# Optimization experiments

Measured on AMD Instinct MI355X. Metric: run time of the kernel, lower is better.

The kernel has to match this reference:

```python
import jax, jax.numpy as jnp
import numpy as np

B, T, E, QKV, H = 2, 2048, 1024, 1024, 16
DH = QKV // H
R_LAYER = 2

def rmsnorm(x):
    eps = jnp.finfo(x.dtype).eps
    return x * jax.lax.rsqrt(jnp.mean(x * x, axis=-1, keepdims=True) + eps)

def w_norm(w, n):
    # scale whole matrix so its (unbiased) std matches n**-0.5
    std = jnp.std(w, ddof=1)
    return w * (n ** -0.5 / (std + 1e-8))

def rotary(x, cos, sin):
    d = x.shape[-1] // 2
    x1, x2 = x[..., :d], x[..., d:]
    return jnp.concatenate([x1 * cos + x2 * sin, -x1 * sin + x2 * cos], axis=-1)

def w_split(w):
    w_qkv = w[:3 * QKV]                               # (3*QKV, E)
    w_sw = w[3 * QKV:5 * QKV].reshape(2 * E, QKV)     # (2*E, QKV)
    w_out = w[5 * QKV:]                               # (E, E)
    return w_qkv, w_sw, w_out

def aft(x, w_qkv):
    qkv = rmsnorm(x) @ w_qkv.T                        # (B,T,3*QKV)
    q, k, v = jnp.split(qkv, 3, axis=-1)
    q, k = rmsnorm(q), rmsnorm(k)
    wexp = jnp.exp(k)
    kv_c = jnp.cumsum(wexp * v, axis=1)
    w_c = jnp.cumsum(wexp, axis=1)
    y = jax.nn.sigmoid(q) * kv_c / (w_c + 1e-6)
    return x, y

def tea(x, cos, sin, w_qkv):
    qkv = (rmsnorm(x) @ w_qkv.T).reshape(B, T, H, 3 * DH)
    q, k, v = jnp.split(qkv, 3, axis=-1)              # each (B,T,H,DH)
    q, k = rotary(q, cos, sin), rotary(k, cos, sin)
    q, k = rmsnorm(q), rmsnorm(k)
    q = q.transpose(0, 2, 1, 3)                       # (B,H,T,DH)
    k = k.transpose(0, 2, 1, 3)
    v = v.transpose(0, 2, 1, 3)
    scores = jnp.einsum('bhqd,bhkd->bhqk', q, k) * DH ** -0.5
    mask = jnp.tril(jnp.ones((T, T), dtype=bool))
    scores = jnp.where(mask, scores, -jnp.inf)
    att = jax.nn.softmax(scores, axis=-1)
    y = jnp.einsum('bhqk,bhkd->bhqd', att, v)
    return x, y.transpose(0, 2, 1, 3).reshape(B, T, QKV)

def swiglu(x, y, w_sw, w_out, ret_oa=True):
    uv = y @ w_sw.T                                   # (B,T,2*E)
    u, v = jnp.split(uv, 2, axis=-1)
    out = x + (u * jax.nn.silu(v)) @ w_out.T
    if not ret_oa:
        return out
    o = rmsnorm(u.reshape(B * T, -1))
    a = v.reshape(B * T, -1)
    oa = jax.nn.softmax((o.T @ a) * E ** -0.5, axis=-1)  # (E,E)
    return out, oa

def setup_inputs():
    key = jax.random.key(0)
    k1, k2 = jax.random.split(key)
    x = jax.random.normal(k1, (B, T, E), dtype=jnp.float32)
    s = 3 ** 0.5 * E ** -0.5
    w = jax.random.uniform(k2, (5 * QKV + E, E), dtype=jnp.float32, minval=-s, maxval=s)
    half = DH // 2
    inv_freq = 1.0 / (10000.0 ** (jnp.arange(half, dtype=jnp.float32) / half))
    freqs = jnp.outer(jnp.arange(T, dtype=jnp.float32), inv_freq)  # (T, half)
    cos = jnp.cos(freqs)[:, None, :]                  # (T,1,half) broadcasts over (B,T,H,half)
    sin = jnp.sin(freqs)[:, None, :]
    return {"x": x, "w": w, "cos": cos, "sin": sin}

def reference(x, w, cos, sin):
    for i in range(R_LAYER):
        w_qkv, w_sw, w_out = w_split(w)
        w_qkv = w_norm(w_qkv, E)
        w_sw = w_norm(w_sw, QKV)
        w_out = w_norm(w_out, E)
        if (i + 1) % 4 == 0:
            x, y = tea(x, cos, sin, w_qkv)
        else:
            x, y = aft(x, w_qkv)
        x, oa = swiglu(x, y, w_sw, w_out, ret_oa=True)
        # RetentionMechanism.forward: hypernetwork weight mixing
        wT = w_norm(w @ oa, 5 * QKV + E)
        w = wT * jax.nn.silu(w) + w
    w_qkv, w_sw, w_out = w_split(w)                   # note: no w_norm on final split (matches source)
    x, y = tea(x, cos, sin, w_qkv)
    return swiglu(x, y, w_sw, w_out, ret_oa=False)
```

## Files before the change

kernel.cpp:

```cpp
#include <hip/hip_runtime.h>
#include <hip/hip_bf16.h>
#include <math.h>

#define TPB 256

constexpr int Bc = 2, Tc = 2048, Ec = 1024, QKVc = 1024, Hc = 16, DHc = 64;
constexpr long BT = (long)Bc * Tc;
constexpr int WR = 5 * QKVc + Ec;
constexpr float F32_EPS = 1.1920928955078125e-07f;
constexpr int NCH = 64, CHL = Tc / NCH;

typedef __attribute__((ext_vector_type(8))) short short8;
typedef __attribute__((ext_vector_type(4))) float f32x4;

__device__ __forceinline__ unsigned short f2bu(float f) {
    union { __hip_bfloat16 h; unsigned short u; } c; c.h = __float2bfloat16(f); return c.u;
}
__device__ __forceinline__ float bu2f(unsigned short u) {
    union { __hip_bfloat16 h; unsigned short u; } c; c.u = u; return __bfloat162float(c.h);
}
__device__ __forceinline__ float ldval(const float* p) { return *p; }
__device__ __forceinline__ float ldval(const unsigned short* p) { return bu2f(*p); }

__device__ __forceinline__ void gload_lds16(const void* g, void* l) {
    __builtin_amdgcn_global_load_lds((const __attribute__((address_space(1))) void*)g,
                                     (__attribute__((address_space(3))) void*)l, 16, 0, 0);
}

template<int CTRL>
__device__ __forceinline__ float dppf(float x) {
    union { float f; int i; } a, b;
    a.f = x;
    b.i = __builtin_amdgcn_update_dpp(0, a.i, CTRL, 0xF, 0xF, true);
    return b.f;
}
__device__ __forceinline__ float max16(float v) {
    v = fmaxf(v, dppf<0xB1>(v));
    v = fmaxf(v, dppf<0x4E>(v));
    v = fmaxf(v, dppf<0x124>(v));
    v = fmaxf(v, dppf<0x128>(v));
    return v;
}
__device__ __forceinline__ float sum16(float v) {
    v += dppf<0xB1>(v);
    v += dppf<0x4E>(v);
    v += dppf<0x124>(v);
    v += dppf<0x128>(v);
    return v;
}

__global__ void k_std_partial3(const float* __restrict__ w, float* __restrict__ out) {
    __shared__ float ls[TPB], lss[TPB];
    int seg = blockIdx.y;
    long base = (seg == 0) ? 0L : (seg == 1 ? 3072L * 1024 : 5120L * 1024);
    long n    = (seg == 0) ? 3072L * 1024 : (seg == 1 ? 2048L * 1024 : 1024L * 1024);
    const float* p = w + base;
    float s = 0.f, ss = 0.f;
    for (long i = (long)blockIdx.x * TPB + threadIdx.x; i < n; i += 256L * TPB) {
        float v = p[i]; s += v; ss += v * v;
    }
    ls[threadIdx.x] = s; lss[threadIdx.x] = ss; __syncthreads();
    for (int o = 128; o > 0; o >>= 1) {
        if (threadIdx.x < o) { ls[threadIdx.x] += ls[threadIdx.x + o]; lss[threadIdx.x] += lss[threadIdx.x + o]; }
        __syncthreads();
    }
    if (threadIdx.x == 0) { out[seg * 512 + blockIdx.x] = ls[0]; out[seg * 512 + 256 + blockIdx.x] = lss[0]; }
}

__global__ void k_std_final3(const float* __restrict__ part, float* __restrict__ scales) {
    __shared__ float ls[TPB], lss[TPB];
    for (int seg = 0; seg < 3; ++seg) {
        ls[threadIdx.x] = part[seg * 512 + threadIdx.x];
        lss[threadIdx.x] = part[seg * 512 + 256 + threadIdx.x];
        __syncthreads();
        for (int o = 128; o > 0; o >>= 1) {
            if (threadIdx.x < o) { ls[threadIdx.x] += ls[threadIdx.x + o]; lss[threadIdx.x] += lss[threadIdx.x + o]; }
            __syncthreads();
        }
        if (threadIdx.x == 0) {
            float n = (seg == 0) ? 3145728.0f : (seg == 1 ? 2097152.0f : 1048576.0f);
            float var = (lss[0] - ls[0] * ls[0] / n) / (n - 1.0f);
            scales[seg] = 0.03125f / (sqrtf(fmaxf(var, 0.0f)) + 1e-8f);
        }
        __syncthreads();
    }
}

__global__ void k_std_partial(const float* __restrict__ p, long n, float* __restrict__ out) {
    __shared__ float ls[TPB], lss[TPB];
    float s = 0.f, ss = 0.f;
    for (long i = (long)blockIdx.x * TPB + threadIdx.x; i < n; i += (long)gridDim.x * TPB) {
        float v = p[i]; s += v; ss += v * v;
    }
    ls[threadIdx.x] = s; lss[threadIdx.x] = ss; __syncthreads();
    for (int o = 128; o > 0; o >>= 1) {
        if (threadIdx.x < o) { ls[threadIdx.x] += ls[threadIdx.x + o]; lss[threadIdx.x] += lss[threadIdx.x + o]; }
        __syncthreads();
    }
    if (threadIdx.x == 0) { out[blockIdx.x] = ls[0]; out[gridDim.x + blockIdx.x] = lss[0]; }
}

__global__ void k_std_final(const float* __restrict__ part, float n, float rs, float* __restrict__ scale) {
    __shared__ float ls[TPB], lss[TPB];
    ls[threadIdx.x] = part[threadIdx.x];
    lss[threadIdx.x] = part[TPB + threadIdx.x];
    __syncthreads();
    for (int o = 128; o > 0; o >>= 1) {
        if (threadIdx.x < o) { ls[threadIdx.x] += ls[threadIdx.x + o]; lss[threadIdx.x] += lss[threadIdx.x + o]; }
        __syncthreads();
    }
    if (threadIdx.x == 0) {
        float var = (lss[0] - ls[0] * ls[0] / n) / (n - 1.0f);
        scale[0] = rs / (sqrtf(fmaxf(var, 0.0f)) + 1e-8f);
    }
}

__global__ void k_rms_qk(unsigned short* __restrict__ qkv) {
    __shared__ float red[TPB];
    int bid = blockIdx.x;
    long row = bid >> 1; int half = bid & 1;
    unsigned short* p = qkv + row * 3072 + half * 1024;
    ushort4 v = *(const ushort4*)(p + threadIdx.x * 4);
    float f0 = bu2f(v.x), f1 = bu2f(v.y), f2 = bu2f(v.z), f3 = bu2f(v.w);
    red[threadIdx.x] = f0 * f0 + f1 * f1 + f2 * f2 + f3 * f3;
    __syncthreads();
    for (int o = 128; o > 0; o >>= 1) {
        if (threadIdx.x < o) red[threadIdx.x] += red[threadIdx.x + o];
        __syncthreads();
    }
    float sc = rsqrtf(red[0] / 1024.0f + F32_EPS);
    ushort4 o4; o4.x = f2bu(f0 * sc); o4.y = f2bu(f1 * sc); o4.z = f2bu(f2 * sc); o4.w = f2bu(f3 * sc);
    *(ushort4*)(p + threadIdx.x * 4) = o4;
}

__global__ void k_rms1024b(const float* __restrict__ in, unsigned short* __restrict__ out, long ldin, long ldout) {
    __shared__ float red[TPB];
    long row = blockIdx.x;
    float4 v = *(const float4*)(in + row * ldin + threadIdx.x * 4);
    float ss = v.x * v.x + v.y * v.y + v.z * v.z + v.w * v.w;
    red[threadIdx.x] = ss; __syncthreads();
    for (int o = 128; o > 0; o >>= 1) {
        if (threadIdx.x < o) red[threadIdx.x] += red[threadIdx.x + o];
        __syncthreads();
    }
    float sc = rsqrtf(red[0] / 1024.0f + F32_EPS);
    ushort4 o4; o4.x = f2bu(v.x * sc); o4.y = f2bu(v.y * sc); o4.z = f2bu(v.z * sc); o4.w = f2bu(v.w * sc);
    *(ushort4*)(out + row * ldout + threadIdx.x * 4) = o4;
}

__global__ void k_cast_bf16(const float* __restrict__ in, unsigned short* __restrict__ out, long n4) {
    long i = (long)blockIdx.x * TPB + threadIdx.x;
    if (i >= n4) return;
    float4 v = *(const float4*)(in + i * 4);
    ushort4 o; o.x = f2bu(v.x); o.y = f2bu(v.y); o.z = f2bu(v.z); o.w = f2bu(v.w);
    *(ushort4*)(out + i * 4) = o;
}

template<typename TI>
__global__ void k_tcast(const TI* __restrict__ in, long ldi, long sIn,
                        unsigned short* __restrict__ out, long ldo, long sOut,
                        const float* __restrict__ rowscale) {
    __shared__ float tile[64][65];
    const TI* ip = in + (long)blockIdx.z * sIn;
    unsigned short* op = out + (long)blockIdx.z * sOut;
    int r0 = blockIdx.y * 64, c0 = blockIdx.x * 64;
    int tid = threadIdx.x;
    int rr = tid >> 4, cc = (tid & 15) * 4;
    #pragma unroll
    for (int u = 0; u < 4; ++u) {
        int r = rr + u * 16;
        float sc = rowscale ? rowscale[r0 + r] : 1.0f;
        #pragma unroll
        for (int j = 0; j < 4; ++j)
            tile[r][cc + j] = ldval(ip + (long)(r0 + r) * ldi + c0 + cc + j) * sc;
    }
    __syncthreads();
    #pragma unroll
    for (int u = 0; u < 4; ++u) {
        int c = rr + u * 16;
        ushort4 o;
        o.x = f2bu(tile[cc + 0][c]); o.y = f2bu(tile[cc + 1][c]);
        o.z = f2bu(tile[cc + 2][c]); o.w = f2bu(tile[cc + 3][c]);
        *(ushort4*)(op + (long)(c0 + c) * ldo + r0 + cc) = o;
    }
}

__global__ void k_tcast2(const unsigned short* __restrict__ uv, const float* __restrict__ uscale,
                         unsigned short* __restrict__ t1, unsigned short* __restrict__ t2) {
    __shared__ float tile[64][65];
    int z = blockIdx.z;
    const unsigned short* ip = uv + (z ? 1024 : 0);
    unsigned short* op = z ? t2 : t1;
    int r0 = blockIdx.y * 64, c0 = blockIdx.x * 64;
    int tid = threadIdx.x;
    int rr = tid >> 4, cc = (tid & 15) * 4;
    #pragma unroll
    for (int u = 0; u < 4; ++u) {
        int r = rr + u * 16;
        float sc = z ? 1.0f : uscale[r0 + r];
        ushort4 v = *(const ushort4*)(ip + (long)(r0 + r) * 2048 + c0 + cc);
        tile[r][cc + 0] = bu2f(v.x) * sc; tile[r][cc + 1] = bu2f(v.y) * sc;
        tile[r][cc + 2] = bu2f(v.z) * sc; tile[r][cc + 3] = bu2f(v.w) * sc;
    }
    __syncthreads();
    #pragma unroll
    for (int u = 0; u < 4; ++u) {
        int c = rr + u * 16;
        ushort4 o;
        o.x = f2bu(tile[cc + 0][c]); o.y = f2bu(tile[cc + 1][c]);
        o.z = f2bu(tile[cc + 2][c]); o.w = f2bu(tile[cc + 3][c]);
        *(ushort4*)(op + (long)(c0 + c) * 4096 + r0 + cc) = o;
    }
}

template<int WRITE_BF16>
__global__ __launch_bounds__(256)
void k_bgemm(int K,
             const unsigned short* __restrict__ A, int lda, long sA,
             const unsigned short* __restrict__ B, int ldb, long sB,
             void* __restrict__ C, int ldc, long sCi, long sSplit, int nsplit,
             const float* __restrict__ scale_ptr, float fscale,
             const float* __restrict__ addp, int ldadd) {
    __shared__ unsigned short Asl[128 * 64];
    __shared__ unsigned short Bsl[128 * 64];
    int bz = blockIdx.z;
    int batch = bz, sp = 0;
    if (nsplit > 1) { batch = bz / nsplit; sp = bz - batch * nsplit; }
    int m0 = blockIdx.y * 128, n0 = blockIdx.x * 128;
    const unsigned short* Ap = A + (long)batch * sA + (long)sp * K;
    const unsigned short* Bp = B + (long)batch * sB + (long)sp * K;
    int tid = threadIdx.x, lane = tid & 63, wave = tid >> 6;
    int wr = wave >> 1, wc = wave & 1;
    f32x4 acc[4][4] = {};
    for (int k0 = 0; k0 < K; k0 += 64) {
        #pragma unroll
        for (int cc = 0; cc < 4; ++cc) {
            int bu = (wave * 4 + cc) * 64;
            int uidx = bu + lane;
            int r = uidx >> 3, slot = uidx & 7;
            int gu = slot ^ (r & 7);
            gload_lds16(Ap + (long)(m0 + r) * lda + k0 + gu * 8, Asl + bu * 8);
        }
        #pragma unroll
        for (int cc = 0; cc < 4; ++cc) {
            int bu = (wave * 4 + cc) * 64;
            int uidx = bu + lane;
            int r = uidx >> 3, slot = uidx & 7;
            int gu = slot ^ (r & 7);
            gload_lds16(Bp + (long)(n0 + r) * ldb + k0 + gu * 8, Bsl + bu * 8);
        }
        __syncthreads();
        #pragma unroll
        for (int ksub = 0; ksub < 2; ++ksub) {
            short8 av[4], bv[4];
            #pragma unroll
            for (int m = 0; m < 4; ++m) {
                int r = wr * 64 + m * 16 + (lane & 15);
                int slot = (ksub * 4 + (lane >> 4)) ^ (r & 7);
                av[m] = *(const short8*)(Asl + r * 64 + slot * 8);
            }
            #pragma unroll
            for (int n = 0; n < 4; ++n) {
                int r = wc * 64 + n * 16 + (lane & 15);
                int slot = (ksub * 4 + (lane >> 4)) ^ (r & 7);
                bv[n] = *(const short8*)(Bsl + r * 64 + slot * 8);
            }
            #pragma unroll
            for (int m = 0; m < 4; ++m)
                #pragma unroll
                for (int n = 0; n < 4; ++n)
                    acc[m][n] = __builtin_amdgcn_mfma_f32_16x16x32_bf16(av[m], bv[n], acc[m][n], 0, 0, 0);
        }
        __syncthreads();
    }
    float s = fscale * (scale_ptr ? scale_ptr[0] : 1.0f);
    long cbase = (long)batch * sCi + (long)sp * sSplit;
    int row0 = m0 + wr * 64, col0 = n0 + wc * 64 + (lane & 15);
    int rbase = (lane >> 4) * 4;
    #pragma unroll
    for (int m = 0; m < 4; ++m)
        #pragma unroll
        for (int i = 0; i < 4; ++i) {
            long row = row0 + m * 16 + rbase + i;
            #pragma unroll
            for (int n = 0; n < 4; ++n) {
                long col = col0 + n * 16;
                float v = acc[m][n][i] * s;
                if (addp) v += addp[row * (long)ldadd + col];
                long idx = cbase + row * ldc + col;
                if (WRITE_BF16) ((unsigned short*)C)[idx] = f2bu(v);
                else ((float*)C)[idx] = v;
            }
        }
}

__global__ __launch_bounds__(256)
void k_flash_split(const unsigned short* __restrict__ hq, const unsigned short* __restrict__ hk,
                   const unsigned short* __restrict__ hvT,
                   unsigned short* __restrict__ opart, float* __restrict__ mpart, float* __restrict__ lpart) {
    __shared__ unsigned short P_lds[4][32 * 136];
    int lane = threadIdx.x & 63, wave = threadIdx.x >> 6;
    unsigned short* P = P_lds[wave];
    int g = lane >> 4, c = lane & 15;
    unsigned bid = blockIdx.x;
    unsigned bswz = (bid & 7) * 160 + (bid >> 3);
    unsigned gi = bswz * 4 + wave;
    unsigned bh = gi / 160, itr = gi % 160;
    int item = 159 - (int)itr;
    int strip, chunk;
    if (item < 16)      { strip = item;                 chunk = 0; }
    else if (item < 48) { strip = 16 + (item - 16) / 2; chunk = (item - 16) & 1; }
    else if (item < 96) { strip = 32 + (item - 48) / 3; chunk = (item - 48) % 3; }
    else                { strip = 48 + (item - 96) / 4; chunk = (item - 96) & 3; }
    int q0 = strip * 32;
    int nt = (q0 + 32 + 127) >> 7;
    int ti0 = chunk * 4;
    int ti1 = ti0 + 4 < nt ? ti0 + 4 : nt;
    const unsigned short* qb = hq + (long)bh * Tc * 64;
    const unsigned short* kb = hk + (long)bh * Tc * 64;
    const unsigned short* vtb = hvT + (long)bh * 64 * Tc;

    short8 qf[2][2];
    #pragma unroll
    for (int mf = 0; mf < 2; ++mf)
        #pragma unroll
        for (int ks = 0; ks < 2; ++ks)
            qf[mf][ks] = *(const short8*)(qb + (long)(q0 + mf * 16 + c) * 64 + ks * 32 + g * 8);

    f32x4 o_acc[2][4] = {};
    float m_run[2][4], lpp[2][4];
    #pragma unroll
    for (int mf = 0; mf < 2; ++mf)
        #pragma unroll
        for (int i = 0; i < 4; ++i) { m_run[mf][i] = -3.0e38f; lpp[mf][i] = 0.f; }

    for (int ti = ti0; ti < ti1; ++ti) {
        int kt = ti * 128;
        short8 vf[4][4];
        #pragma unroll
        for (int ks2 = 0; ks2 < 4; ++ks2)
            #pragma unroll
            for (int df = 0; df < 4; ++df)
                vf[ks2][df] = *(const short8*)(vtb + (long)(df * 16 + c) * Tc + kt + ks2 * 32 + g * 8);
        f32x4 s_acc[2][8] = {};
        #pragma unroll
        for (int ks = 0; ks < 2; ++ks) {
            short8 kf[8];
            #pragma unroll
            for (int nf = 0; nf < 8; ++nf)
                kf[nf] = *(const short8*)(kb + (long)(kt + nf * 16 + c) * 64 + ks * 32 + g * 8);
            #pragma unroll
            for (int mf = 0; mf < 2; ++mf)
                #pragma unroll
                for (int nf = 0; nf < 8; ++nf)
                    s_acc[mf][nf] = __builtin_amdgcn_mfma_f32_16x16x32_bf16(qf[mf][ks], kf[nf], s_acc[mf][nf], 0, 0, 0);
        }
        if (ti == nt - 1) {
            #pragma unroll
            for (int mf = 0; mf < 2; ++mf)
                #pragma unroll
                for (int nf = 0; nf < 8; ++nf)
                    #pragma unroll
                    for (int i = 0; i < 4; ++i)
                        if ((kt + nf * 16 + c) > (q0 + mf * 16 + g * 4 + i)) s_acc[mf][nf][i] = -1.0e30f;
        }
        float pm[2][4];
        #pragma unroll
        for (int mf = 0; mf < 2; ++mf)
            #pragma unroll
            for (int i = 0; i < 4; ++i) {
                float a = fmaxf(fmaxf(s_acc[mf][0][i], s_acc[mf][1][i]),
                                fmaxf(s_acc[mf][2][i], s_acc[mf][3][i]));
                float b = fmaxf(fmaxf(s_acc[mf][4][i], s_acc[mf][5][i]),
                                fmaxf(s_acc[mf][6][i], s_acc[mf][7][i]));
                pm[mf][i] = max16(fmaxf(a, b));
            }
        float mg = 0.f;
        #pragma unroll
        for (int mf = 0; mf < 2; ++mf)
            #pragma unroll
            for (int i = 0; i < 4; ++i) {
                pm[mf][i] *= 0.125f;
                mg = fmaxf(mg, pm[mf][i] - m_run[mf][i]);
            }
        if (__any(mg > 8.0f)) {
            #pragma unroll
            for (int mf = 0; mf < 2; ++mf)
                #pragma unroll
                for (int i = 0; i < 4; ++i) {
                    float mn = fmaxf(m_run[mf][i], pm[mf][i]);
                    float corr = __expf(m_run[mf][i] - mn);
                    m_run[mf][i] = mn;
                    lpp[mf][i] *= corr;
                    #pragma unroll
                    for (int df = 0; df < 4; ++df) o_acc[mf][df][i] *= corr;
                }
        }
        #pragma unroll
        for (int mf = 0; mf < 2; ++mf)
            #pragma unroll
            for (int nf = 0; nf < 8; ++nf)
                #pragma unroll
                for (int i = 0; i < 4; ++i) {
                    float p = __expf(fmaf(s_acc[mf][nf][i], 0.125f, -m_run[mf][i]));
                    P[(mf * 16 + g * 4 + i) * 136 + nf * 16 + c] = f2bu(p);
                    lpp[mf][i] += p;
                }
        #pragma unroll
        for (int ks2 = 0; ks2 < 4; ++ks2) {
            short8 pa[2];
            #pragma unroll
            for (int mf = 0; mf < 2; ++mf)
                pa[mf] = *(const short8*)(P + (mf * 16 + c) * 136 + ks2 * 32 + g * 8);
            #pragma unroll
            for (int mf = 0; mf < 2; ++mf)
                #pragma unroll
                for (int df = 0; df < 4; ++df)
                    o_acc[mf][df] = __builtin_amdgcn_mfma_f32_16x16x32_bf16(pa[mf], vf[ks2][df], o_acc[mf][df], 0, 0, 0);
        }
    }
    #pragma unroll
    for (int mf = 0; mf < 2; ++mf)
        #pragma unroll
        for (int i = 0; i < 4; ++i)
            lpp[mf][i] = sum16(lpp[mf][i]);
    long pbase = (long)(bh * 160 + item);
    #pragma unroll
    for (int mf = 0; mf < 2; ++mf)
        #pragma unroll
        for (int i = 0; i < 4; ++i) {
            int row_l = mf * 16 + g * 4 + i;
            #pragma unroll
            for (int df = 0; df < 4; ++df)
                opart[pbase * 2048 + row_l * 64 + df * 16 + c] = f2bu(o_acc[mf][df][i]);
            if (c == 0) {
                mpart[pbase * 32 + row_l] = m_run[mf][i];
                lpart[pbase * 32 + row_l] = lpp[mf][i];
            }
        }
}

__global__ __launch_bounds__(256)
void k_flash_merge(const unsigned short* __restrict__ opart, const float* __restrict__ mpart,
                   const float* __restrict__ lpart, unsigned short* __restrict__ yout) {
    int bs = blockIdx.x;
    int bh = bs >> 6, strip = bs & 63;
    int b = bh >> 4, h = bh & 15;
    int np, base;
    if (strip < 16)      { np = 1; base = strip; }
    else if (strip < 32) { np = 2; base = 16 + (strip - 16) * 2; }
    else if (strip < 48) { np = 3; base = 48 + (strip - 32) * 3; }
    else                 { np = 4; base = 96 + (strip - 48) * 4; }
    long p0 = (long)(bh * 160 + base);
    int tid = threadIdx.x;
    int r = tid >> 3, c0 = (tid & 7) * 8;
    float M = -3.0e38f;
    for (int p = 0; p < np; ++p) M = fmaxf(M, mpart[(p0 + p) * 32 + r]);
    float L = 0.f;
    float acc[8] = {};
    for (int p = 0; p < np; ++p) {
        float sc = __expf(mpart[(p0 + p) * 32 + r] - M);
        L += lpart[(p0 + p) * 32 + r] * sc;
        const unsigned short* op = opart + (p0 + p) * 2048 + r * 64 + c0;
        ushort4 a = *(const ushort4*)op;
        ushort4 bq = *(const ushort4*)(op + 4);
        acc[0] += bu2f(a.x) * sc; acc[1] += bu2f(a.y) * sc;
        acc[2] += bu2f(a.z) * sc; acc[3] += bu2f(a.w) * sc;
        acc[4] += bu2f(bq.x) * sc; acc[5] += bu2f(bq.y) * sc;
        acc[6] += bu2f(bq.z) * sc; acc[7] += bu2f(bq.w) * sc;
    }
    float inv = 1.0f / L;
    long row = (long)b * Tc + strip * 32 + r;
    unsigned short* yp = yout + row * 1024 + h * 64 + c0;
    ushort4 o1, o2;
    o1.x = f2bu(acc[0] * inv); o1.y = f2bu(acc[1] * inv); o1.z = f2bu(acc[2] * inv); o1.w = f2bu(acc[3] * inv);
    o2.x = f2bu(acc[4] * inv); o2.y = f2bu(acc[5] * inv); o2.z = f2bu(acc[6] * inv); o2.w = f2bu(acc[7] * inv);
    *(ushort4*)yp = o1;
    *(ushort4*)(yp + 4) = o2;
}

__global__ void k_aft_p1(const unsigned short* __restrict__ qkv, float* __restrict__ cw, float* __restrict__ cs) {
    int id = blockIdx.x * TPB + threadIdx.x;
    int bc = id & 2047, ch = id >> 11;
    int b = bc >> 10, c = bc & 1023;
    const unsigned short* base = qkv + ((long)(b * Tc + ch * CHL)) * 3072 + c;
    float sw = 0.f, sv = 0.f;
    for (int i = 0; i < CHL; ++i) {
        float k = bu2f(base[1024]), v = bu2f(base[2048]);
        float e = __expf(k);
        sw += e; sv += e * v;
        base += 3072;
    }
    cw[ch * 2048 + bc] = sw; cs[ch * 2048 + bc] = sv;
}

__global__ void k_aft_p3(const unsigned short* __restrict__ qkv, const float* __restrict__ cw,
                         const float* __restrict__ cs, unsigned short* __restrict__ y) {
    int id = blockIdx.x * TPB + threadIdx.x;
    int bc = id & 2047, ch = id >> 11;
    int b = bc >> 10, c = bc & 1023;
    float aw = 0.f, av = 0.f;
    for (int cc = 0; cc < ch; ++cc) { aw += cw[cc * 2048 + bc]; av += cs[cc * 2048 + bc]; }
    long t0 = (long)b * Tc + ch * CHL;
    const unsigned short* base = qkv + t0 * 3072 + c;
    unsigned short* yp = y + t0 * 1024 + c;
    for (int i = 0; i < CHL; ++i) {
        float q = bu2f(base[0]), k = bu2f(base[1024]), v = bu2f(base[2048]);
        float e = __expf(k);
        av += e * v; aw += e;
        float sig = 1.0f / (1.0f + __expf(-q));
        yp[0] = f2bu(sig * av / (aw + 1e-6f));
        base += 3072; yp += 1024;
    }
}

__global__ void k_silu_rms(const unsigned short* __restrict__ uv, unsigned short* __restrict__ g,
                           float* __restrict__ rs) {
    __shared__ float red[TPB];
    long row = blockIdx.x;
    const unsigned short* up = uv + row * 2048;
    ushort4 u4 = *(const ushort4*)(up + threadIdx.x * 4);
    ushort4 v4 = *(const ushort4*)(up + 1024 + threadIdx.x * 4);
    float u0 = bu2f(u4.x), u1 = bu2f(u4.y), u2 = bu2f(u4.z), u3 = bu2f(u4.w);
    float v0 = bu2f(v4.x), v1 = bu2f(v4.y), v2 = bu2f(v4.z), v3 = bu2f(v4.w);
    ushort4 o;
    o.x = f2bu(u0 * v0 / (1.f + __expf(-v0)));
    o.y = f2bu(u1 * v1 / (1.f + __expf(-v1)));
    o.z = f2bu(u2 * v2 / (1.f + __expf(-v2)));
    o.w = f2bu(u3 * v3 / (1.f + __expf(-v3)));
    *(ushort4*)(g + row * 1024 + threadIdx.x * 4) = o;
    red[threadIdx.x] = u0 * u0 + u1 * u1 + u2 * u2 + u3 * u3;
    __syncthreads();
    for (int off = 128; off > 0; off >>= 1) {
        if (threadIdx.x < off) red[threadIdx.x] += red[threadIdx.x + off];
        __syncthreads();
    }
    if (threadIdx.x == 0) rs[row] = rsqrtf(red[0] / 1024.0f + F32_EPS);
}

__global__ void k_silu_gate(const unsigned short* __restrict__ uv, unsigned short* __restrict__ g, long n4) {
    long i = (long)blockIdx.x * TPB + threadIdx.x;
    if (i >= n4) return;
    long r = i >> 8, c4 = i & 255;
    ushort4 u4 = *(const ushort4*)(uv + r * 2048 + c4 * 4);
    ushort4 v4 = *(const ushort4*)(uv + r * 2048 + 1024 + c4 * 4);
    float u0 = bu2f(u4.x), u1 = bu2f(u4.y), u2 = bu2f(u4.z), u3 = bu2f(u4.w);
    float v0 = bu2f(v4.x), v1 = bu2f(v4.y), v2 = bu2f(v4.z), v3 = bu2f(v4.w);
    ushort4 o;
    o.x = f2bu(u0 * v0 / (1.f + __expf(-v0)));
    o.y = f2bu(u1 * v1 / (1.f + __expf(-v1)));
    o.z = f2bu(u2 * v2 / (1.f + __expf(-v2)));
    o.w = f2bu(u3 * v3 / (1.f + __expf(-v3)));
    *(ushort4*)(g + r * 1024 + c4 * 4) = o;
}

__global__ void k_wupdate(float* __restrict__ wout, const float* __restrict__ win,
                          const float* __restrict__ p, const float* __restrict__ scale,
                          unsigned short* __restrict__ wb, long n4) {
    long i = (long)blockIdx.x * TPB + threadIdx.x;
    if (i >= n4) return;
    float s = scale[0];
    float4 wv = *(const float4*)(win + i * 4);
    float4 pv = *(const float4*)(p + i * 4);
    float4 o;
    o.x = pv.x * s * (wv.x / (1.f + __expf(-wv.x))) + wv.x;
    o.y = pv.y * s * (wv.y / (1.f + __expf(-wv.y))) + wv.y;
    o.z = pv.z * s * (wv.z / (1.f + __expf(-wv.z))) + wv.z;
    o.w = pv.w * s * (wv.w / (1.f + __expf(-wv.w))) + wv.w;
    *(float4*)(wout + i * 4) = o;
    ushort4 ob; ob.x = f2bu(o.x); ob.y = f2bu(o.y); ob.z = f2bu(o.z); ob.w = f2bu(o.w);
    *(ushort4*)(wb + i * 4) = ob;
}

__global__ void k_softmax4(const float* __restrict__ parts, float* __restrict__ outb, float fscale) {
    __shared__ float red[TPB];
    __shared__ float rowbuf[1024];
    long row = blockIdx.x;
    const float* p0 = parts + row * 1024;
    for (int c = threadIdx.x; c < 1024; c += TPB) {
        float v = p0[c] + p0[c + 1048576] + p0[c + 2097152] + p0[c + 3145728];
        rowbuf[c] = v * fscale;
    }
    __syncthreads();
    float m = -3.0e38f;
    for (int c = threadIdx.x; c < 1024; c += TPB) m = fmaxf(m, rowbuf[c]);
    red[threadIdx.x] = m; __syncthreads();
    for (int o = 128; o > 0; o >>= 1) {
        if (threadIdx.x < o) red[threadIdx.x] = fmaxf(red[threadIdx.x], red[threadIdx.x + o]);
        __syncthreads();
    }
    m = red[0]; __syncthreads();
    float sum = 0.f;
    for (int c = threadIdx.x; c < 1024; c += TPB) sum += __expf(rowbuf[c] - m);
    red[threadIdx.x] = sum; __syncthreads();
    for (int o = 128; o > 0; o >>= 1) {
        if (threadIdx.x < o) red[threadIdx.x] += red[threadIdx.x + o];
        __syncthreads();
    }
    float inv = 1.0f / red[0];
    for (int c = threadIdx.x; c < 1024; c += TPB)
        outb[row * 1024 + c] = __expf(rowbuf[c] - m) * inv;
}

__global__ void k_rot_split(const unsigned short* __restrict__ qkvp, const float* __restrict__ cosp,
                            const float* __restrict__ sinp, unsigned short* __restrict__ hq,
                            unsigned short* __restrict__ hk, unsigned short* __restrict__ hv) {
    __shared__ float row[3072];
    __shared__ float cs[32], sn[32];
    int bt = blockIdx.x;
    int b = bt >> 11, t = bt & 2047;
    const unsigned short* src = qkvp + (long)bt * 3072;
    #pragma unroll
    for (int u = 0; u < 3; ++u) {
        int idx = threadIdx.x + u * 256;
        ushort4 v = *(const ushort4*)(src + idx * 4);
        row[idx * 4 + 0] = bu2f(v.x); row[idx * 4 + 1] = bu2f(v.y);
        row[idx * 4 + 2] = bu2f(v.z); row[idx * 4 + 3] = bu2f(v.w);
    }
    if (threadIdx.x < 32) { cs[threadIdx.x] = cosp[t * 32 + threadIdx.x]; sn[threadIdx.x] = sinp[t * 32 + threadIdx.x]; }
    __syncthreads();
    int h = threadIdx.x >> 4, li = threadIdx.x & 15;
    int base = h * 192;
    long obase = ((long)(b * Hc + h) * Tc + t) * 64 + li * 4;
    {
        float r[4]; float ss = 0.f;
        #pragma unroll
        for (int j = 0; j < 4; ++j) {
            int d = li * 4 + j;
            float val = (d < 32) ? (row[base + d] * cs[d] + row[base + d + 32] * sn[d])
                                 : (-row[base + d - 32] * sn[d - 32] + row[base + d] * cs[d - 32]);
            r[j] = val; ss += val * val;
        }
        ss = sum16(ss);
        float sc = rsqrtf(ss / 64.0f + F32_EPS);
        ushort4 o; o.x = f2bu(r[0] * sc); o.y = f2bu(r[1] * sc); o.z = f2bu(r[2] * sc); o.w = f2bu(r[3] * sc);
        *(ushort4*)(hq + obase) = o;
    }
    {
        int kb = base + 64;
        float r[4]; float ss = 0.f;
        #pragma unroll
        for (int j = 0; j < 4; ++j) {
            int d = li * 4 + j;
            float val = (d < 32) ? (row[kb + d] * cs[d] + row[kb + d + 32] * sn[d])
                                 : (-row[kb + d - 32] * sn[d - 32] + row[kb + d] * cs[d - 32]);
            r[j] = val; ss += val * val;
        }
        ss = sum16(ss);
        float sc = rsqrtf(ss / 64.0f + F32_EPS);
        ushort4 o; o.x = f2bu(r[0] * sc); o.y = f2bu(r[1] * sc); o.z = f2bu(r[2] * sc); o.w = f2bu(r[3] * sc);
        *(ushort4*)(hk + obase) = o;
    }
    {
        ushort4 o;
        o.x = f2bu(row[base + 128 + li * 4 + 0]); o.y = f2bu(row[base + 128 + li * 4 + 1]);
        o.z = f2bu(row[base + 128 + li * 4 + 2]); o.w = f2bu(row[base + 128 + li * 4 + 3]);
        *(ushort4*)(hv + obase) = o;
    }
}

extern "C" void kernel_launch(void* const* d_in, const int* in_sizes, int n_in,
                              void* d_out, int out_size, void* d_ws, size_t ws_size,
                              hipStream_t stream) {
    const float* x_in = (const float*)d_in[0];
    const float* w_in = (const float*)d_in[1];
    const float* cos_in = (const float*)d_in[2];
    const float* sin_in = (const float*)d_in[3];
    float* out = (float*)d_out;
    float* ws = (float*)d_ws;

    long off = 0;
    float* w_cur = ws + off;  off += (long)WR * Ec;
    float* w_tmp = ws + off;  off += (long)WR * Ec;
    float* xbuf  = ws + off;  off += BT * Ec;
    float* R     = ws + off;  off += BT * 3L * QKVc;
    float* oab   = ws + off;  off += (long)Ec * Ec;
    float* red   = ws + off;  off += 2048;
    float* scales= ws + off;  off += 16;
    float* uscale= ws + off;  off += 4096;
    float* chw   = ws + off;  off += 2048L * NCH;
    float* chs   = ws + off;  off += 2048L * NCH;
    unsigned short* qkvb  = (unsigned short*)R;
    unsigned short* uvb   = qkvb + 12582912L;
    unsigned short* opartb= qkvb;
    float* mpart = oab;
    float* lpart = oab + 5120L * 32;

    unsigned short* bp = (unsigned short*)(ws + off);
    long bo = 0;
    unsigned short* wb  = bp + bo; bo += (long)WR * Ec;
    unsigned short* xbn = bp + bo; bo += BT * Ec;
    unsigned short* ybn = bp + bo; bo += BT * Ec;
    unsigned short* gbn = bp + bo; bo += BT * Ec;
    unsigned short* t1  = bp + bo; bo += BT * Ec;
    unsigned short* t2  = bp + bo; bo += BT * Ec;
    unsigned short* t3  = bp + bo; bo += BT * Ec;
    unsigned short* t4  = bp + bo; bo += BT * Ec;

    const float rsWR = 1.0f / sqrtf(6144.0f);
    const long wsw = 3072L * 1024, wout = 5120L * 1024;

    k_cast_bf16<<<(int)(((long)WR * Ec / 4) / TPB), TPB, 0, stream>>>(w_in, wb, (long)WR * Ec / 4);

    for (int layer = 0; layer < 2; ++layer) {
        const float* wsrc = layer == 0 ? w_in : w_cur;
        const float* xsrc = layer == 0 ? x_in : xbuf;
        k_std_partial3<<<dim3(256, 3), TPB, 0, stream>>>(wsrc, red);
        k_std_final3<<<1, TPB, 0, stream>>>(red, scales);
        k_rms1024b<<<BT, TPB, 0, stream>>>(xsrc, xbn, 1024, 1024);
        k_bgemm<1><<<dim3(24, 32, 1), TPB, 0, stream>>>(
            1024, xbn, 1024, 0, wb, 1024, 0, qkvb, 3072, 0, 0, 1, scales + 0, 1.0f, nullptr, 0);
        k_rms_qk<<<8192, TPB, 0, stream>>>(qkvb);
        k_aft_p1<<<(2048 * NCH) / TPB, TPB, 0, stream>>>(qkvb, chw, chs);
        k_aft_p3<<<(2048 * NCH) / TPB, TPB, 0, stream>>>(qkvb, chw, chs, ybn);
        k_bgemm<1><<<dim3(16, 32, 1), TPB, 0, stream>>>(
            1024, ybn, 1024, 0, wb + wsw, 1024, 0, uvb, 2048, 0, 0, 1, scales + 1, 1.0f, nullptr, 0);
        k_silu_rms<<<BT, TPB, 0, stream>>>(uvb, gbn, uscale);
        k_tcast2<<<dim3(16, 64, 2), TPB, 0, stream>>>(uvb, uscale, t1, t2);
        k_bgemm<0><<<dim3(8, 8, 4), TPB, 0, stream>>>(
            1024, t1, 4096, 0, t2, 4096, 0, w_tmp, 1024, 0, 1048576L, 4, nullptr, 1.0f, nullptr, 0);
        k_softmax4<<<1024, TPB, 0, stream>>>(w_tmp, oab, 0.03125f);
        k_tcast<float><<<dim3(16, 16, 1), TPB, 0, stream>>>(oab, 1024, 0, t3, 1024, 0, nullptr);
        k_bgemm<0><<<dim3(8, 32, 1), TPB, 0, stream>>>(
            1024, gbn, 1024, 0, wb + wout, 1024, 0, xbuf, 1024, 0, 0, 1, scales + 2, 1.0f, xsrc, 1024);
        k_bgemm<0><<<dim3(8, 48, 1), TPB, 0, stream>>>(
            1024, wb, 1024, 0, t3, 1024, 0, w_tmp, 1024, 0, 0, 1, nullptr, 1.0f, nullptr, 0);
        k_std_partial<<<256, TPB, 0, stream>>>(w_tmp, (long)WR * 1024, red);
        k_std_final<<<1, TPB, 0, stream>>>(red, (float)((long)WR * 1024), rsWR, scales + 3);
        k_wupdate<<<(int)(((long)WR * 1024 / 4) / TPB), TPB, 0, stream>>>(
            w_cur, wsrc, w_tmp, scales + 3, wb, (long)WR * 1024 / 4);
    }

    k_rms1024b<<<BT, TPB, 0, stream>>>(xbuf, xbn, 1024, 1024);
    k_bgemm<1><<<dim3(24, 32, 1), TPB, 0, stream>>>(
        1024, xbn, 1024, 0, wb, 1024, 0, qkvb, 3072, 0, 0, 1, nullptr, 1.0f, nullptr, 0);
    k_rot_split<<<BT, TPB, 0, stream>>>(qkvb, cos_in, sin_in, t1, t2, t3);
    k_tcast<unsigned short><<<dim3(1, 32, 32), TPB, 0, stream>>>(
        t3, 64, (long)Tc * 64, t4, 2048, (long)Tc * 64, nullptr);
    k_flash_split<<<dim3(1280), TPB, 0, stream>>>(t1, t2, t4, opartb, mpart, lpart);
    k_flash_merge<<<dim3(2048), TPB, 0, stream>>>(opartb, mpart, lpart, ybn);
    k_bgemm<1><<<dim3(16, 32, 1), TPB, 0, stream>>>(
        1024, ybn, 1024, 0, wb + wsw, 1024, 0, uvb, 2048, 0, 0, 1, nullptr, 1.0f, nullptr, 0);
    k_silu_gate<<<(int)((BT * 1024 / 4) / TPB), TPB, 0, stream>>>(uvb, gbn, BT * 1024 / 4);
    k_bgemm<0><<<dim3(8, 32, 1), TPB, 0, stream>>>(
        1024, gbn, 1024, 0, wb + wout, 1024, 0, out, 1024, 0, 0, 1, nullptr, 1.0f, xbuf, 1024);
}
```

Measured before the change: 832.1 us.

## Halve flash key tile to 64 and prefetch next K tile in registers

The split flash-attention kernel now processes 64-key tiles instead of 128, with twice as many tiles per chunk so each chunk covers the same range. K fragments for the next tile are loaded into registers while the current tile's softmax and PV MFMAs run, overlapping global loads with compute. The smaller tile also cuts per-wave register pressure and LDS for P, but it doubles the per-tile overhead of the max reduction and rescale checks.

```diff
diff --git a/kernel.cpp b/kernel.cpp
--- a/kernel.cpp
+++ b/kernel.cpp
@@ -298,7 +298,7 @@
 void k_flash_split(const unsigned short* __restrict__ hq, const unsigned short* __restrict__ hk,
                    const unsigned short* __restrict__ hvT,
                    unsigned short* __restrict__ opart, float* __restrict__ mpart, float* __restrict__ lpart) {
-    __shared__ unsigned short P_lds[4][32 * 136];
+    __shared__ unsigned short P_lds[4][32 * 72];
     int lane = threadIdx.x & 63, wave = threadIdx.x >> 6;
     unsigned short* P = P_lds[wave];
     int g = lane >> 4, c = lane & 15;
@@ -313,9 +313,9 @@
     else if (item < 96) { strip = 32 + (item - 48) / 3; chunk = (item - 48) % 3; }
     else                { strip = 48 + (item - 96) / 4; chunk = (item - 96) & 3; }
     int q0 = strip * 32;
-    int nt = (q0 + 32 + 127) >> 7;
-    int ti0 = chunk * 4;
-    int ti1 = ti0 + 4 < nt ? ti0 + 4 : nt;
+    int nt = (q0 + 32 + 63) >> 6;
+    int ti0 = chunk * 8;
+    int ti1 = ti0 + 8 < nt ? ti0 + 8 : nt;
     const unsigned short* qb = hq + (long)bh * Tc * 64;
     const unsigned short* kb = hk + (long)bh * Tc * 64;
     const unsigned short* vtb = hvT + (long)bh * 64 * Tc;
@@ -334,32 +334,44 @@
         #pragma unroll
         for (int i = 0; i < 4; ++i) { m_run[mf][i] = -3.0e38f; lpp[mf][i] = 0.f; }
 
+    short8 kcur[2][4];
+    #pragma unroll
+    for (int ks = 0; ks < 2; ++ks)
+        #pragma unroll
+        for (int nf = 0; nf < 4; ++nf)
+            kcur[ks][nf] = *(const short8*)(kb + (long)(ti0 * 64 + nf * 16 + c) * 64 + ks * 32 + g * 8);
+
     for (int ti = ti0; ti < ti1; ++ti) {
-        int kt = ti * 128;
-        short8 vf[4][4];
-        #pragma unroll
-        for (int ks2 = 0; ks2 < 4; ++ks2)
+        int kt = ti * 64;
+        short8 vf[2][4];
+        #pragma unroll
+        for (int ks = 0; ks < 2; ++ks)
             #pragma unroll
             for (int df = 0; df < 4; ++df)
-                vf[ks2][df] = *(const short8*)(vtb + (long)(df * 16 + c) * Tc + kt + ks2 * 32 + g * 8);
-        f32x4 s_acc[2][8] = {};
-        #pragma unroll
-        for (int ks = 0; ks < 2; ++ks) {
-            short8 kf[8];
-            #pragma unroll
-            for (int nf = 0; nf < 8; ++nf)
-                kf[nf] = *(const short8*)(kb + (long)(kt + nf * 16 + c) * 64 + ks * 32 + g * 8);
+                vf[ks][df] = *(const short8*)(vtb + (long)(df * 16 + c) * Tc + kt + ks * 32 + g * 8);
+        f32x4 s_acc[2][4] = {};
+        #pragma unroll
+        for (int ks = 0; ks < 2; ++ks)
             #pragma unroll
             for (int mf = 0; mf < 2; ++mf)
                 #pragma unroll
-                for (int nf = 0; nf < 8; ++nf)
-                    s_acc[mf][nf] = __builtin_amdgcn_mfma_f32_16x16x32_bf16(qf[mf][ks], kf[nf], s_acc[mf][nf], 0, 0, 0);
+                for (int nf = 0; nf < 4; ++nf)
+                    s_acc[mf][nf] = __builtin_amdgcn_mfma_f32_16x16x32_bf16(qf[mf][ks], kcur[ks][nf], s_acc[mf][nf], 0, 0, 0);
+        short8 knxt[2][4];
+        bool more = (ti + 1 < ti1);
+        if (more) {
+            int kt2 = kt + 64;
+            #pragma unroll
+            for (int ks = 0; ks < 2; ++ks)
+                #pragma unroll
+                for (int nf = 0; nf < 4; ++nf)
+                    knxt[ks][nf] = *(const short8*)(kb + (long)(kt2 + nf * 16 + c) * 64 + ks * 32 + g * 8);
         }
         if (ti == nt - 1) {
             #pragma unroll
             for (int mf = 0; mf < 2; ++mf)
                 #pragma unroll
-                for (int nf = 0; nf < 8; ++nf)
+                for (int nf = 0; nf < 4; ++nf)
                     #pragma unroll
                     for (int i = 0; i < 4; ++i)
                         if ((kt + nf * 16 + c) > (q0 + mf * 16 + g * 4 + i)) s_acc[mf][nf][i] = -1.0e30f;
@@ -368,13 +380,9 @@
         #pragma unroll
         for (int mf = 0; mf < 2; ++mf)
             #pragma unroll
-            for (int i = 0; i < 4; ++i) {
-                float a = fmaxf(fmaxf(s_acc[mf][0][i], s_acc[mf][1][i]),
-                                fmaxf(s_acc[mf][2][i], s_acc[mf][3][i]));
-                float b = fmaxf(fmaxf(s_acc[mf][4][i], s_acc[mf][5][i]),
-                                fmaxf(s_acc[mf][6][i], s_acc[mf][7][i]));
-                pm[mf][i] = max16(fmaxf(a, b));
-            }
+            for (int i = 0; i < 4; ++i)
+                pm[mf][i] = max16(fmaxf(fmaxf(s_acc[mf][0][i], s_acc[mf][1][i]),
+                                        fmaxf(s_acc[mf][2][i], s_acc[mf][3][i])));
         float mg = 0.f;
         #pragma unroll
         for (int mf = 0; mf < 2; ++mf)
@@ -399,24 +407,31 @@
         #pragma unroll
         for (int mf = 0; mf < 2; ++mf)
             #pragma unroll
-            for (int nf = 0; nf < 8; ++nf)
+            for (int nf = 0; nf < 4; ++nf)
                 #pragma unroll
                 for (int i = 0; i < 4; ++i) {
                     float p = __expf(fmaf(s_acc[mf][nf][i], 0.125f, -m_run[mf][i]));
-                    P[(mf * 16 + g * 4 + i) * 136 + nf * 16 + c] = f2bu(p);
+                    P[(mf * 16 + g * 4 + i) * 72 + nf * 16 + c] = f2bu(p);
                     lpp[mf][i] += p;
                 }
         #pragma unroll
-        for (int ks2 = 0; ks2 < 4; ++ks2) {
+        for (int ks = 0; ks < 2; ++ks) {
             short8 pa[2];
             #pragma unroll
             for (int mf = 0; mf < 2; ++mf)
-                pa[mf] = *(const short8*)(P + (mf * 16 + c) * 136 + ks2 * 32 + g * 8);
+                pa[mf] = *(const short8*)(P + (mf * 16 + c) * 72 + ks * 32 + g * 8);
             #pragma unroll
             for (int mf = 0; mf < 2; ++mf)
                 #pragma unroll
                 for (int df = 0; df < 4; ++df)
-                    o_acc[mf][df] = __builtin_amdgcn_mfma_f32_16x16x32_bf16(pa[mf], vf[ks2][df], o_acc[mf][df], 0, 0, 0);
+                    o_acc[mf][df] = __builtin_amdgcn_mfma_f32_16x16x32_bf16(pa[mf], vf[ks][df], o_acc[mf][df], 0, 0, 0);
+        }
+        if (more) {
+            #pragma unroll
+            for (int ks = 0; ks < 2; ++ks)
+                #pragma unroll
+                for (int nf = 0; nf < 4; ++nf)
+                    kcur[ks][nf] = knxt[ks][nf];
         }
     }
     #pragma unroll
```

After: 825.9 us. About the same (-0.7%).
